# Kernel optimization log

Hardware: AMD Instinct MI355X
Metric: run time of the kernel (lower is better)

## Reference

```python
import jax, jax.numpy as jnp
import numpy as np

N = 50000
F = 256
E = 800000


def setup_inputs() -> dict:
    key = jax.random.key(0)
    k1, k2, k3, k4 = jax.random.split(key, 4)
    H = jax.random.normal(k1, (N, F), dtype=jnp.float32)
    H0 = jax.random.normal(k2, (N, F), dtype=jnp.float32)
    # edge list for sparse adjacency: row 0 = i (row index), row 1 = j (col index)
    edge_index = jax.random.randint(k3, (2, E), 0, N, dtype=jnp.int32)
    # W ~ U(-stdv, stdv), stdv = 1/sqrt(out_features), as in reset_parameters
    stdv = 1.0 / np.sqrt(F)
    W = jax.random.uniform(k4, (F, F), minval=-stdv, maxval=stdv, dtype=jnp.float32)
    lamda = jnp.float32(0.5)
    alpha = jnp.float32(0.1)
    l = 4
    return {"H": H, "edge_index": edge_index, "H0": H0, "W": W,
            "lamda": lamda, "alpha": alpha, "l": l}


def reference(H, edge_index, H0, W, lamda, alpha, l):
    n = H.shape[0]
    src = edge_index[0]  # i: row index of A[i, j]
    dst = edge_index[1]  # j: col index
    # A_hat = A + I ; degree = column sums of A_hat (tf.reduce_sum(A_hat, 0))
    deg = jax.ops.segment_sum(jnp.ones(src.shape[0], dtype=H.dtype), dst,
                              num_segments=n) + 1.0
    d_inv_sqrt = jax.lax.rsqrt(deg)
    # (P H)_i = d_i^{-1/2} * sum_j A[i,j] d_j^{-1/2} H_j  +  H_i / d_i  (self loop)
    msg = H[dst] * d_inv_sqrt[dst][:, None]            # [E, F]
    agg = jax.ops.segment_sum(msg, src, num_segments=n)  # [N, F]
    PH = d_inv_sqrt[:, None] * agg + H / deg[:, None]
    init_res = (1.0 - alpha) * PH + alpha * H0
    beta = jnp.log(lamda / l + 1.0)
    # init_res @ ((1-beta) I + beta W)
    output = (1.0 - beta) * init_res + beta * (init_res @ W)
    return output
```

## Files before the change

### kernel.cpp

```cpp
#include <hip/hip_runtime.h>
#include <math.h>


#define F_DIM 256
#define CHUNK 20000

typedef __attribute__((ext_vector_type(4))) float f32x4;
typedef __attribute__((ext_vector_type(8))) short short8;
typedef __attribute__((ext_vector_type(4))) unsigned short u16x4;

static __device__ __forceinline__ unsigned short f2bf(float f) {
    unsigned int u = __float_as_uint(f);
    u += 0x7fffu + ((u >> 16) & 1u);
    return (unsigned short)(u >> 16);
}
static __device__ __forceinline__ float bf2f(unsigned short u) {
    return __uint_as_float((unsigned int)u << 16);
}


__global__ __launch_bounds__(1024) void hist_kernel(
        const int* __restrict__ src, const int* __restrict__ dst,
        unsigned* __restrict__ histS, unsigned* __restrict__ histD,
        unsigned char* __restrict__ lrank, int E, int wpc4) {
    __shared__ unsigned hist[12544];
    int b = blockIdx.x;
    int which = b & 1, c = b >> 1;
    int tid = threadIdx.x;
    int e0 = c * CHUNK;
    int e1 = e0 + CHUNK < E ? e0 + CHUNK : E;
    const int* eptr = which ? dst : src;
    unsigned* outh = which ? histD : histS;

    for (int w = tid; w < wpc4; w += 1024) hist[w] = 0;
    __syncthreads();
    for (int e = e0 + tid; e < e1; e += 1024) {
        int s = eptr[e];
        int sh = (s & 3) * 8;
        unsigned old = atomicAdd(&hist[s >> 2], 1u << sh);
        if (!which) lrank[e] = (unsigned char)((old >> sh) & 0xffu);
    }
    __syncthreads();
    for (int w = tid; w < wpc4; w += 1024)
        outh[(size_t)c * wpc4 + w] = hist[w];
}


__global__ __launch_bounds__(256) void sumbase_kernel(
        const unsigned* __restrict__ histS, const unsigned* __restrict__ histD,
        int* __restrict__ cnt, float* __restrict__ dinv,
        unsigned* __restrict__ baseL, int* __restrict__ blksum,
        int wpc4, int nchunk, int n) {
    int tid = threadIdx.x;
    int w = blockIdx.x * 256 + tid;
    unsigned s0 = 0, s1 = 0, s2 = 0, s3 = 0;
    unsigned d0 = 0, d1 = 0, d2 = 0, d3 = 0;
    if (w < wpc4) {
        for (int c = 0; c < nchunk; ++c) {
            unsigned vs = histS[(size_t)c * wpc4 + w];
            unsigned vd = histD[(size_t)c * wpc4 + w];
            baseL[(size_t)c * wpc4 + w] = s0 | (s1 << 8) | (s2 << 16) | (s3 << 24);
            s0 += vs & 0xffu; s1 += (vs >> 8) & 0xffu;
            s2 += (vs >> 16) & 0xffu; s3 += vs >> 24;
            d0 += vd & 0xffu; d1 += (vd >> 8) & 0xffu;
            d2 += (vd >> 16) & 0xffu; d3 += vd >> 24;
        }
        int i0 = 4 * w;
        unsigned sv[4] = {s0, s1, s2, s3};
        unsigned dv[4] = {d0, d1, d2, d3};
        for (int k = 0; k < 4; ++k) {
            if (i0 + k < n) {
                cnt[i0 + k] = (int)sv[k];
                dinv[i0 + k] = rsqrtf((float)dv[k] + 1.0f);
            }
        }
    }
    int contrib = (w < wpc4) ? (int)(s0 + s1 + s2 + s3) : 0;
    int lane = tid & 63, wid = tid >> 6;
    int v = contrib;
    for (int off = 32; off > 0; off >>= 1) v += __shfl_down(v, off, 64);
    if (lane == 0) blksum[4 * blockIdx.x + wid] = v;
}


__global__ __launch_bounds__(256) void rowptr_kernel(const int* __restrict__ cnt,
                                                     const int* __restrict__ blksum,
                                                     int* __restrict__ row_ptr,
                                                     int n, int nb) {
    int tid = threadIdx.x;
    int lane = tid & 63, w = tid >> 6;
    int bv = (tid < nb) ? blksum[tid] : 0;
    int bs = bv;
    for (int off = 1; off < 64; off <<= 1) {
        int t = __shfl_up(bv, off, 64);
        if (lane >= off) bv += t;
    }
    __shared__ int wsb[4];
    __shared__ int sbo[256];
    if (lane == 63) wsb[w] = bv;
    __syncthreads();
    if (tid == 0) {
        int run = 0;
        for (int k = 0; k < 4; ++k) { int t = wsb[k]; wsb[k] = run; run += t; }
    }
    __syncthreads();
    sbo[tid] = wsb[w] + bv - bs;
    __syncthreads();
    int blockoff = sbo[blockIdx.x];
    int i = blockIdx.x * 256 + tid;
    int s = (i < n) ? cnt[i] : 0;
    int v = s;
    for (int off = 1; off < 64; off <<= 1) {
        int t = __shfl_up(v, off, 64);
        if (lane >= off) v += t;
    }
    __shared__ int ws[4];
    if (lane == 63) ws[w] = v;
    __syncthreads();
    if (tid == 0) {
        int run = 0;
        for (int k = 0; k < 4; ++k) { int t = ws[k]; ws[k] = run; run += t; }
    }
    __syncthreads();
    if (i <= n) row_ptr[i] = blockoff + ws[w] + v - s;
}


__global__ __launch_bounds__(256) void fillhswt_kernel(
        const int* __restrict__ src, const int* __restrict__ dst,
        const int* __restrict__ row_ptr, const unsigned char* __restrict__ baseL8,
        const unsigned char* __restrict__ lrank, int* __restrict__ col,
        const float* __restrict__ H, const float* __restrict__ dinv,
        unsigned short* __restrict__ Hs,
        const float* __restrict__ W, unsigned short* __restrict__ Wt,
        const float* __restrict__ lamda_p, const int* __restrict__ l_p,
        int E, int wpc4, int nfill, int total4) {
    int bid = blockIdx.x;
    int tid = threadIdx.x;
    if (bid < nfill) {
        int e = bid * 256 + tid;
        if (e < E) {
            int c = e / CHUNK;
            int s = src[e];
            unsigned lb = baseL8[(size_t)c * (4 * wpc4) + s];
            unsigned pos = (unsigned)row_ptr[s] + lb + lrank[e];
            col[pos] = dst[e];
        }
    } else {
        int i = (bid - nfill) * 256 + tid;
        if (i < total4) {
            int row = i >> 6;
            float d = dinv[row];
            f32x4 x = ((const f32x4*)H)[i];
            u16x4 o;
            o[0] = f2bf(x[0] * d); o[1] = f2bf(x[1] * d);
            o[2] = f2bf(x[2] * d); o[3] = f2bf(x[3] * d);
            ((u16x4*)Hs)[i] = o;
        } else {
            int t = i - total4;
            if (t < F_DIM * F_DIM) {
                float beta = logf(lamda_p[0] / (float)l_p[0] + 1.0f);
                int nn = t >> 8, kk = t & 255;
                float v = beta * W[kk * F_DIM + nn];
                if (kk == nn) v += 1.0f - beta;
                Wt[nn * F_DIM + kk] = f2bf(v);
            }
        }
    }
}


#define ACC(A, h) { A[0] += bf2f(h[0]); A[1] += bf2f(h[1]); \
                    A[2] += bf2f(h[2]); A[3] += bf2f(h[3]); }

__global__ __launch_bounds__(256) void gather_kernel(
        const unsigned short* __restrict__ Hs,
        const int* __restrict__ row_ptr, const int* __restrict__ col,
        const float* __restrict__ dinv,
        unsigned short* __restrict__ phb, int n) {
    int wave = threadIdx.x >> 6;
    int lane = threadIdx.x & 63;
    int row = blockIdx.x * 4 + wave;
    if (row >= n) return;
    const u16x4* Hs4 = (const u16x4*)Hs;

    int beg = row_ptr[row], end = row_ptr[row + 1];
    f32x4 a0 = 0.0f, a1 = 0.0f, a2 = 0.0f, a3 = 0.0f;
    int e = beg;
    for (; e + 8 <= end; e += 8) {
        int j0 = col[e+0], j1 = col[e+1], j2 = col[e+2], j3 = col[e+3];
        int j4 = col[e+4], j5 = col[e+5], j6 = col[e+6], j7 = col[e+7];
        u16x4 h0 = Hs4[j0*64+lane], h1 = Hs4[j1*64+lane];
        u16x4 h2 = Hs4[j2*64+lane], h3 = Hs4[j3*64+lane];
        u16x4 h4 = Hs4[j4*64+lane], h5 = Hs4[j5*64+lane];
        u16x4 h6 = Hs4[j6*64+lane], h7 = Hs4[j7*64+lane];
        ACC(a0, h0) ACC(a1, h1) ACC(a2, h2) ACC(a3, h3)
        ACC(a0, h4) ACC(a1, h5) ACC(a2, h6) ACC(a3, h7)
    }
    for (; e + 4 <= end; e += 4) {
        int j0 = col[e+0], j1 = col[e+1], j2 = col[e+2], j3 = col[e+3];
        u16x4 h0 = Hs4[j0*64+lane], h1 = Hs4[j1*64+lane];
        u16x4 h2 = Hs4[j2*64+lane], h3 = Hs4[j3*64+lane];
        ACC(a0, h0) ACC(a1, h1) ACC(a2, h2) ACC(a3, h3)
    }
    for (; e < end; ++e) {
        int j = col[e];
        u16x4 h = Hs4[j*64+lane];
        ACC(a0, h)
    }
    u16x4 hr = Hs4[row*64+lane];
    ACC(a2, hr)
    f32x4 acc = (a0 + a1) + (a2 + a3);
    float di = dinv[row];
    f32x4 ph = di * acc;
    u16x4 o;
    o[0] = f2bf(ph[0]); o[1] = f2bf(ph[1]);
    o[2] = f2bf(ph[2]); o[3] = f2bf(ph[3]);
    __builtin_nontemporal_store(o, (u16x4*)phb + row * 64 + lane);
}


__global__ __launch_bounds__(256) void gemm_kernel(
        const unsigned short* __restrict__ phb, const float* __restrict__ H0,
        const unsigned short* __restrict__ Wt, float* __restrict__ out,
        const float* __restrict__ alpha_p, int M) {
    int w = threadIdx.x >> 6;
    int mr = blockIdx.x * 64;
    int nc = w * 64;
    int lane = threadIdx.x & 63;
    int lo = lane & 15, hi = lane >> 4;
    float alpha = alpha_p[0], oma = 1.0f - alpha;

    f32x4 acc[4][4] = {};
    for (int kk = 0; kk < 8; ++kk) {
        int kb = kk * 32 + hi * 8;
        short8 a[4], b[4];
        for (int am = 0; am < 4; ++am) {
            int row = mr + am * 16 + lo;
            if (row < M) {
                size_t base = (size_t)row * F_DIM + kb;
                short8 p = *(const short8*)(phb + base);
                f32x4 x0 = *(const f32x4*)(H0 + base);
                f32x4 x1 = *(const f32x4*)(H0 + base + 4);
                short8 t;
                t[0] = (short)f2bf(oma * bf2f((unsigned short)p[0]) + alpha * x0[0]);
                t[1] = (short)f2bf(oma * bf2f((unsigned short)p[1]) + alpha * x0[1]);
                t[2] = (short)f2bf(oma * bf2f((unsigned short)p[2]) + alpha * x0[2]);
                t[3] = (short)f2bf(oma * bf2f((unsigned short)p[3]) + alpha * x0[3]);
                t[4] = (short)f2bf(oma * bf2f((unsigned short)p[4]) + alpha * x1[0]);
                t[5] = (short)f2bf(oma * bf2f((unsigned short)p[5]) + alpha * x1[1]);
                t[6] = (short)f2bf(oma * bf2f((unsigned short)p[6]) + alpha * x1[2]);
                t[7] = (short)f2bf(oma * bf2f((unsigned short)p[7]) + alpha * x1[3]);
                a[am] = t;
            } else {
                a[am] = (short8)0;
            }
        }
        for (int bn = 0; bn < 4; ++bn) {
            int cb = nc + bn * 16 + lo;
            b[bn] = *(const short8*)(Wt + cb * F_DIM + kb);
        }
        for (int am = 0; am < 4; ++am)
            for (int bn = 0; bn < 4; ++bn)
                acc[am][bn] = __builtin_amdgcn_mfma_f32_16x16x32_bf16(
                    a[am], b[bn], acc[am][bn], 0, 0, 0);
    }

    for (int am = 0; am < 4; ++am) {
        int rbase = mr + am * 16 + hi * 4;
        for (int r = 0; r < 4; ++r) {
            int row = rbase + r;
            if (row >= M) continue;
            for (int bn = 0; bn < 4; ++bn) {
                int c2 = nc + bn * 16 + lo;
                out[(size_t)row * F_DIM + c2] = acc[am][bn][r];
            }
        }
    }
}


extern "C" void kernel_launch(void* const* d_in, const int* in_sizes, int n_in,
                              void* d_out, int out_size, void* d_ws, size_t ws_size,
                              hipStream_t stream) {
    const float* H     = (const float*)d_in[0];
    const int*   ei    = (const int*)d_in[1];
    const float* H0    = (const float*)d_in[2];
    const float* W     = (const float*)d_in[3];
    const float* lamda = (const float*)d_in[4];
    const float* alpha = (const float*)d_in[5];
    const int*   lp    = (const int*)d_in[6];

    int n = in_sizes[0] / F_DIM;
    int E = in_sizes[1] / 2;
    const int* src = ei;
    const int* dst = ei + E;
    float* out = (float*)d_out;

    int wpc4 = (n + 3) / 4;
    int nchunk = (E + CHUNK - 1) / CHUNK;
    int nb = (n + 256) / 256;

    char* ws = (char*)d_ws;
    size_t off = 0;
    auto alloc = [&](size_t bytes) -> void* {
        void* p = ws + off;
        off += (bytes + 255) & ~(size_t)255;
        return p;
    };
    unsigned* histS = (unsigned*)alloc((size_t)nchunk * wpc4 * 4);
    unsigned* histD = (unsigned*)alloc((size_t)nchunk * wpc4 * 4);
    unsigned* baseL = (unsigned*)alloc((size_t)nchunk * wpc4 * 4);
    unsigned char* lrank = (unsigned char*)alloc((size_t)E);
    int* cnt     = (int*)alloc((size_t)n * 4);
    int* row_ptr = (int*)alloc(((size_t)n + 1) * 4);
    int* blksum  = (int*)alloc((size_t)(nb + 8) * 4);
    float* dinv  = (float*)alloc((size_t)n * 4);
    int* colb    = (int*)alloc((size_t)E * 4);
    unsigned short* Wt  = (unsigned short*)alloc((size_t)F_DIM * F_DIM * 2);
    unsigned short* Hs  = (unsigned short*)alloc((size_t)n * F_DIM * 2);
    unsigned short* phb = (unsigned short*)alloc(((size_t)n + 64) * F_DIM * 2);

    hist_kernel<<<nchunk * 2, 1024, 0, stream>>>(src, dst, histS, histD, lrank,
                                                 E, wpc4);
    int wgrid = (wpc4 + 255) / 256;
    sumbase_kernel<<<wgrid, 256, 0, stream>>>(histS, histD, cnt, dinv, baseL,
                                              blksum, wpc4, nchunk, n);
    rowptr_kernel<<<nb, 256, 0, stream>>>(cnt, blksum, row_ptr, n, nb);
    int nfill = (E + 255) / 256;
    int total4 = n * 64;
    int nhswt = (total4 + F_DIM * F_DIM + 255) / 256;
    fillhswt_kernel<<<nfill + nhswt, 256, 0, stream>>>(
        src, dst, row_ptr, (const unsigned char*)baseL, lrank, colb,
        H, dinv, Hs, W, Wt, lamda, lp, E, wpc4, nfill, total4);
    gather_kernel<<<(n + 3) / 4, 256, 0, stream>>>(Hs, row_ptr, colb, dinv,
                                                   phb, n);
    int mtiles = (n + 63) / 64;
    gemm_kernel<<<mtiles, 256, 0, stream>>>(phb, H0, Wt, out, alpha, n);
}
```

Before: 181.6 us.

## Stage blended A tile in LDS once per block instead of per-wave global reloads

The GEMM kernel now loads the 64x256 block of phb and H0 cooperatively with coalesced vector loads, applies the alpha blend and bf16 conversion once, and stores the result in padded shared memory. Each of the four waves then reads its MFMA A operands from LDS. Before, every wave reloaded and reconverted the same A rows from global memory, a fourfold redundancy. The SpMM output store is also changed from nontemporal to a normal store so phb can stay in cache for the GEMM. In exchange the GEMM uses about 33 KB of LDS per block and a barrier, which may lower occupancy and stops global loads from overlapping with MFMA work.

```diff
diff --git a/kernel.cpp b/kernel.cpp
--- a/kernel.cpp
+++ b/kernel.cpp
@@ -216,7 +216,7 @@
     u16x4 o;
     o[0] = f2bf(ph[0]); o[1] = f2bf(ph[1]);
     o[2] = f2bf(ph[2]); o[3] = f2bf(ph[3]);
-    __builtin_nontemporal_store(o, (u16x4*)phb + row * 64 + lane);
+    ((u16x4*)phb)[row * 64 + lane] = o;
 }
 
 
@@ -224,38 +224,41 @@
         const unsigned short* __restrict__ phb, const float* __restrict__ H0,
         const unsigned short* __restrict__ Wt, float* __restrict__ out,
         const float* __restrict__ alpha_p, int M) {
-    int w = threadIdx.x >> 6;
+    __shared__ __align__(16) unsigned short At[64][264];
+    int tid = threadIdx.x;
     int mr = blockIdx.x * 64;
+    float alpha = alpha_p[0], oma = 1.0f - alpha;
+
+    for (int i = tid; i < 4096; i += 256) {
+        int row = i >> 6, wc = i & 63;
+        int grow = mr + row;
+        u16x4 o;
+        if (grow < M) {
+            size_t base = (size_t)grow * F_DIM + wc * 4;
+            u16x4 p = *(const u16x4*)(phb + base);
+            f32x4 x = *(const f32x4*)(H0 + base);
+            o[0] = f2bf(oma * bf2f(p[0]) + alpha * x[0]);
+            o[1] = f2bf(oma * bf2f(p[1]) + alpha * x[1]);
+            o[2] = f2bf(oma * bf2f(p[2]) + alpha * x[2]);
+            o[3] = f2bf(oma * bf2f(p[3]) + alpha * x[3]);
+        } else {
+            o = (u16x4)0;
+        }
+        *(u16x4*)&At[row][wc * 4] = o;
+    }
+    __syncthreads();
+
+    int w = tid >> 6;
     int nc = w * 64;
-    int lane = threadIdx.x & 63;
+    int lane = tid & 63;
     int lo = lane & 15, hi = lane >> 4;
-    float alpha = alpha_p[0], oma = 1.0f - alpha;
 
     f32x4 acc[4][4] = {};
     for (int kk = 0; kk < 8; ++kk) {
         int kb = kk * 32 + hi * 8;
         short8 a[4], b[4];
-        for (int am = 0; am < 4; ++am) {
-            int row = mr + am * 16 + lo;
-            if (row < M) {
-                size_t base = (size_t)row * F_DIM + kb;
-                short8 p = *(const short8*)(phb + base);
-                f32x4 x0 = *(const f32x4*)(H0 + base);
-                f32x4 x1 = *(const f32x4*)(H0 + base + 4);
-                short8 t;
-                t[0] = (short)f2bf(oma * bf2f((unsigned short)p[0]) + alpha * x0[0]);
-                t[1] = (short)f2bf(oma * bf2f((unsigned short)p[1]) + alpha * x0[1]);
-                t[2] = (short)f2bf(oma * bf2f((unsigned short)p[2]) + alpha * x0[2]);
-                t[3] = (short)f2bf(oma * bf2f((unsigned short)p[3]) + alpha * x0[3]);
-                t[4] = (short)f2bf(oma * bf2f((unsigned short)p[4]) + alpha * x1[0]);
-                t[5] = (short)f2bf(oma * bf2f((unsigned short)p[5]) + alpha * x1[1]);
-                t[6] = (short)f2bf(oma * bf2f((unsigned short)p[6]) + alpha * x1[2]);
-                t[7] = (short)f2bf(oma * bf2f((unsigned short)p[7]) + alpha * x1[3]);
-                a[am] = t;
-            } else {
-                a[am] = (short8)0;
-            }
-        }
+        for (int am = 0; am < 4; ++am)
+            a[am] = *(const short8*)&At[am * 16 + lo][kb];
         for (int bn = 0; bn < 4; ++bn) {
             int cb = nc + bn * 16 + lo;
             b[bn] = *(const short8*)(Wt + cb * F_DIM + kb);
```

After: 159.3 us. -12.3%, faster.
